# Kernel tuning notes

Hardware: AMD Instinct MI355X
Metric: run time of the kernel (lower is better)

## Reference

```python
import jax, jax.numpy as jnp
import numpy as np

N = 64000            # total nodes (64 graphs x 1000 nodes)
E = 1048576          # edges (~16 avg degree)
NB_NODES = 1000
NUM_GRAPHS = 64
F_IN, H1, H2, H3, OUT = 128, 256, 256, 128, 64


def setup_inputs() -> dict:
    key = jax.random.key(0)
    ks = jax.random.split(key, 12)
    x = jax.random.normal(ks[0], (N, F_IN), dtype=jnp.float32)
    # random edges within each graph: pick graph per edge, then local src/dst
    g = jax.random.randint(ks[1], (E,), 0, NUM_GRAPHS)
    src = g * NB_NODES + jax.random.randint(ks[2], (E,), 0, NB_NODES)
    dst = g * NB_NODES + jax.random.randint(ks[3], (E,), 0, NB_NODES)
    edge_index = jnp.stack([src, dst]).astype(jnp.int64)
    batch = (jnp.arange(N) // NB_NODES).astype(jnp.int64)  # sorted graph ids
    def glorot(k, fan_in, fan_out):
        s = jnp.sqrt(6.0 / (fan_in + fan_out))
        return jax.random.uniform(k, (fan_in, fan_out), jnp.float32, -s, s)
    return {
        "x": x, "edge_index": edge_index, "batch": batch,
        "W1": glorot(ks[4], F_IN, H1), "b1": jnp.zeros((H1,), jnp.float32),
        "W2": glorot(ks[5], H1, H2),   "b2": jnp.zeros((H2,), jnp.float32),
        "W3": glorot(ks[6], H2, H3),   "b3": jnp.zeros((H3,), jnp.float32),
        "Wfc": glorot(ks[7], H3 * NB_NODES, OUT),
        "bfc": jnp.zeros((OUT,), jnp.float32),
    }


def _gcn_norm(edge_index, n):
    # add self-loops, symmetric normalization D^-1/2 (A+I) D^-1/2
    loop = jnp.arange(n, dtype=edge_index.dtype)
    src = jnp.concatenate([edge_index[0], loop])
    dst = jnp.concatenate([edge_index[1], loop])
    deg = jax.ops.segment_sum(jnp.ones_like(src, jnp.float32), dst, num_segments=n)
    dinv = 1.0 / jnp.sqrt(deg)  # deg >= 1 thanks to self-loops
    norm = dinv[src] * dinv[dst]
    return src, dst, norm


def _gcn_layer(h, W, b, src, dst, norm, n):
    hl = h @ W                                   # [N, H]
    msg = hl[src] * norm[:, None]                # gather + scale
    agg = jax.ops.segment_sum(msg, dst, num_segments=n)  # scatter-add
    return agg + b


def reference(x, edge_index, batch, W1, b1, W2, b2, W3, b3, Wfc, bfc):
    n = x.shape[0]
    src, dst, norm = _gcn_norm(edge_index, n)
    h = jnp.tanh(_gcn_layer(x, W1, b1, src, dst, norm, n))
    h = jnp.tanh(_gcn_layer(h, W2, b2, src, dst, norm, n))
    h = jnp.tanh(_gcn_layer(h, W3, b3, src, dst, norm, n))
    # batch is sorted with equal graph sizes -> the per-graph loop/concat
    # in the original is exactly a reshape to [num_graphs, nodes*H3]
    h_concat = h.reshape(NUM_GRAPHS, NB_NODES * H3)
    return h_concat @ Wfc + bfc
```

## Files before the change

kernel.cpp:

```cpp
#include <hip/hip_runtime.h>
#include <math.h>

#define N_NODES 64000
#define N_EDGES 1048576
#define NB 1000
#define NG 64
#define NOUT 64
#define FC_SPLIT 500
#define BK_CAP 18000

typedef __attribute__((ext_vector_type(8))) short bfrag;
typedef __attribute__((ext_vector_type(4))) float f32x4;
typedef __attribute__((ext_vector_type(2))) float f32x2;

__device__ inline float bflo(unsigned int u) {
    union { unsigned int i; float f; } x; x.i = u << 16; return x.f;
}
__device__ inline float bfhi(unsigned int u) {
    union { unsigned int i; float f; } x; x.i = u & 0xffff0000u; return x.f;
}
__device__ inline f32x2 upk(unsigned int u) {
    f32x2 r; r.x = bflo(u); r.y = bfhi(u); return r;
}
__device__ inline unsigned short f2bf(float f) {
    union { float f; unsigned int i; } x; x.f = f;
    return (unsigned short)((x.i + 0x7FFFu + ((x.i >> 16) & 1u)) >> 16);
}
__device__ inline float tanh_fast(float x) {
    float e = __expf(2.0f * x);
    return fmaf(-2.0f, __builtin_amdgcn_rcpf(e + 1.0f), 1.0f);
}
__device__ inline int swz32(int row, int g) { return g ^ (row & 7) ^ (g >> 3); }
__device__ inline int swz16(int row, int g) { return g ^ (row & 7) ^ (g >> 3); }


__global__ __launch_bounds__(256) void k_bucket(const int* __restrict__ src,
                                                const int* __restrict__ dst,
                                                int* __restrict__ gcnt,
                                                unsigned int* __restrict__ bucket) {
    __shared__ int lcnt[64];
    __shared__ int lbase[64];
    __shared__ int lcur[64];
    int t = threadIdx.x;
    int e0 = blockIdx.x * 4096;
    if (t < 64) { lcnt[t] = 0; lcur[t] = 0; }
    __syncthreads();
    for (int i = t; i < 4096; i += 256) {
        int d = dst[e0 + i];
        int g = d / NB;
        atomicAdd(&lcnt[g], 1);
    }
    __syncthreads();
    if (t < 64) lbase[t] = atomicAdd(&gcnt[t], lcnt[t]);
    __syncthreads();
    for (int i = t; i < 4096; i += 256) {
        int d = dst[e0 + i];
        int s = src[e0 + i];
        int g = d / NB;
        int pos = atomicAdd(&lcur[g], 1);
        unsigned int packed = ((unsigned int)(d - g * NB) << 10) | (unsigned int)(s - g * NB);
        bucket[(size_t)g * BK_CAP + lbase[g] + pos] = packed;
    }
}

__global__ __launch_bounds__(1024) void k_build(const int* __restrict__ gcnt,
                                                const unsigned int* __restrict__ bucket,
                                                int* __restrict__ rowptr,
                                                int* __restrict__ rowend,
                                                float* __restrict__ dinv,
                                                unsigned short* __restrict__ colp) {
    __shared__ int ind[1024];
    __shared__ int tmp[1024];
    int t = threadIdx.x;
    int g = blockIdx.x;
    int cnt = gcnt[g];
    size_t base = (size_t)g * BK_CAP;
    ind[t] = 0;
    __syncthreads();
    for (int i = t; i < cnt; i += 1024) {
        unsigned int p = bucket[base + i];
        atomicAdd(&ind[p >> 10], 1);
    }
    __syncthreads();
    int deg = ind[t];
    if (t < NB) dinv[g * NB + t] = rsqrtf((float)(deg + 1));
    tmp[t] = deg;
    __syncthreads();
    for (int off = 1; off < 1024; off <<= 1) {
        int o = (t >= off) ? tmp[t - off] : 0;
        __syncthreads();
        tmp[t] += o;
        __syncthreads();
    }
    int excl = tmp[t] - deg;
    if (t < NB) {
        rowptr[g * NB + t] = (int)base + excl;
        rowend[g * NB + t] = (int)base + excl + deg;
    }
    ind[t] = excl;
    __syncthreads();
    for (int i = t; i < cnt; i += 1024) {
        unsigned int p = bucket[base + i];
        int dl = p >> 10;
        int pos = atomicAdd(&ind[dl], 1);
        colp[base + pos] = (unsigned short)(p & 1023u);
    }
}


__global__ void k_cast_scale(const float* __restrict__ in, const float* __restrict__ dinv,
                             unsigned short* __restrict__ out) {
    int i = (blockIdx.x * blockDim.x + threadIdx.x) * 4;
    float d = dinv[i >> 7];
    float4 v = *(const float4*)(in + i);
    union { unsigned short s[4]; uint2 u; } o;
    o.s[0] = f2bf(v.x * d); o.s[1] = f2bf(v.y * d);
    o.s[2] = f2bf(v.z * d); o.s[3] = f2bf(v.w * d);
    *(uint2*)(out + i) = o.u;
}

__global__ void k_wt_all(const float* __restrict__ W1, const float* __restrict__ W2,
                         const float* __restrict__ W3, unsigned short* __restrict__ W1t,
                         unsigned short* __restrict__ W2t, unsigned short* __restrict__ W3t) {
    int i = blockIdx.x * 256 + threadIdx.x;
    if (i < 32768) {
        int n = i / 128, k = i % 128;
        W1t[i] = f2bf(W1[k * 256 + n]);
    } else if (i < 98304) {
        int j = i - 32768;
        int n = j / 256, k = j % 256;
        W2t[j] = f2bf(W2[k * 256 + n]);
    } else {
        int j = i - 98304;
        int n = j / 256, k = j % 256;
        W3t[j] = f2bf(W3[k * 128 + n]);
    }
}


template <int H, bool TANH>
__global__ __launch_bounds__(256) void k_agg(const unsigned short* __restrict__ hs,
                                             unsigned short* __restrict__ op,
                                             const int* __restrict__ rowptr,
                                             const int* __restrict__ rowend,
                                             const unsigned short* __restrict__ col,
                                             const float* __restrict__ dinv,
                                             const float* __restrict__ bias) {
    constexpr int VEC = H / 64;
    int lane = threadIdx.x & 63;
    int b = blockIdx.x;
    int c = b & 7;
    int j = b >> 3;
    int g = c + 8 * (j / 250);
    int chunk = j % 250;
    int v = g * NB + chunk * 4 + (threadIdx.x >> 6);
    const unsigned short* gb = hs + (size_t)g * NB * H;
    f32x2 a0, a1;
    a0 = f32x2{0.f, 0.f}; a1 = f32x2{0.f, 0.f};
    {
        const unsigned short* r = hs + (size_t)v * H + lane * VEC;
        if (VEC == 2) {
            a0 = upk(*(const unsigned int*)r);
        } else {
            uint2 u = *(const uint2*)r;
            a0 = upk(u.x); a1 = upk(u.y);
        }
    }
    int beg = rowptr[v], end = rowend[v];
    for (int e0 = beg; e0 < end; e0 += 64) {
        int me = e0 + lane;
        int s = (me < end) ? (int)col[me] : 0;
        int cnt = min(64, end - e0);
        int i = 0;
        for (; i + 8 <= cnt; i += 8) {
            int sx[8];
#pragma unroll
            for (int q = 0; q < 8; ++q) sx[q] = __builtin_amdgcn_readlane(s, i + q);
            if (VEC == 2) {
                unsigned int u[8];
#pragma unroll
                for (int q = 0; q < 8; ++q)
                    u[q] = *(const unsigned int*)(gb + (size_t)sx[q] * H + lane * 2);
#pragma unroll
                for (int q = 0; q < 8; ++q) a0 += upk(u[q]);
            } else {
                uint2 u[8];
#pragma unroll
                for (int q = 0; q < 8; ++q)
                    u[q] = *(const uint2*)(gb + (size_t)sx[q] * H + lane * 4);
#pragma unroll
                for (int q = 0; q < 8; ++q) { a0 += upk(u[q].x); a1 += upk(u[q].y); }
            }
        }
        for (; i + 4 <= cnt; i += 4) {
            int sx[4];
#pragma unroll
            for (int q = 0; q < 4; ++q) sx[q] = __builtin_amdgcn_readlane(s, i + q);
            if (VEC == 2) {
                unsigned int u[4];
#pragma unroll
                for (int q = 0; q < 4; ++q)
                    u[q] = *(const unsigned int*)(gb + (size_t)sx[q] * H + lane * 2);
#pragma unroll
                for (int q = 0; q < 4; ++q) a0 += upk(u[q]);
            } else {
                uint2 u[4];
#pragma unroll
                for (int q = 0; q < 4; ++q)
                    u[q] = *(const uint2*)(gb + (size_t)sx[q] * H + lane * 4);
#pragma unroll
                for (int q = 0; q < 4; ++q) { a0 += upk(u[q].x); a1 += upk(u[q].y); }
            }
        }
        for (; i < cnt; ++i) {
            int ss = __builtin_amdgcn_readlane(s, i);
            if (VEC == 2) {
                a0 += upk(*(const unsigned int*)(gb + (size_t)ss * H + lane * 2));
            } else {
                uint2 u = *(const uint2*)(gb + (size_t)ss * H + lane * 4);
                a0 += upk(u.x); a1 += upk(u.y);
            }
        }
    }
    float dv = dinv[v];
    float acc[4];
    acc[0] = a0.x; acc[1] = a0.y;
    if (VEC == 4) { acc[2] = a1.x; acc[3] = a1.y; }
    if (TANH) {
#pragma unroll
        for (int q = 0; q < VEC; ++q) acc[q] = tanh_fast(acc[q] * dv + bias[lane * VEC + q]);
    } else {
#pragma unroll
        for (int q = 0; q < VEC; ++q) acc[q] *= dv;
    }
    unsigned short* o = op + (size_t)v * H + lane * VEC;
    if (VEC == 2) {
        union { unsigned short s[2]; unsigned int u; } pk;
        pk.s[0] = f2bf(acc[0]); pk.s[1] = f2bf(acc[1]);
        *(unsigned int*)o = pk.u;
    } else {
        union { unsigned short s[4]; uint2 u; } pk;
        pk.s[0] = f2bf(acc[0]); pk.s[1] = f2bf(acc[1]);
        pk.s[2] = f2bf(acc[2]); pk.s[3] = f2bf(acc[3]);
        *(uint2*)o = pk.u;
    }
}


__global__ __launch_bounds__(256, 4) void k_aggemm1(const unsigned short* __restrict__ P0,
                                                    const int* __restrict__ rowptr,
                                                    const int* __restrict__ rowend,
                                                    const unsigned short* __restrict__ col,
                                                    const float* __restrict__ dinv,
                                                    const unsigned short* __restrict__ W1t,
                                                    const float* __restrict__ b1,
                                                    unsigned short* __restrict__ C) {
    constexpr int K = 128, N = 256;
    __shared__ unsigned short at[32 * 128];
    int t = threadIdx.x;
    int w = t >> 6, l = t & 63;
    int lm = l & 15, lq = l >> 4;
    int n0 = w * 64;
    int row0 = lq * 4;
    int m0 = blockIdx.x * 32;

    for (int r = 0; r < 8; ++r) {
        int row = w * 8 + r;
        int v = m0 + row;
        int gv = v / NB;
        const unsigned short* gb = P0 + (size_t)gv * NB * K;
        f32x2 a0 = upk(*(const unsigned int*)(P0 + (size_t)v * K + l * 2));
        int beg = rowptr[v], end = rowend[v];
        for (int e0 = beg; e0 < end; e0 += 64) {
            int me = e0 + l;
            int s = (me < end) ? (int)col[me] : 0;
            int cnt = min(64, end - e0);
            int i = 0;
            for (; i + 8 <= cnt; i += 8) {
                int sx[8];
#pragma unroll
                for (int q = 0; q < 8; ++q) sx[q] = __builtin_amdgcn_readlane(s, i + q);
                unsigned int u[8];
#pragma unroll
                for (int q = 0; q < 8; ++q)
                    u[q] = *(const unsigned int*)(gb + (size_t)sx[q] * K + l * 2);
#pragma unroll
                for (int q = 0; q < 8; ++q) a0 += upk(u[q]);
            }
            for (; i + 4 <= cnt; i += 4) {
                int sx[4];
#pragma unroll
                for (int q = 0; q < 4; ++q) sx[q] = __builtin_amdgcn_readlane(s, i + q);
                unsigned int u[4];
#pragma unroll
                for (int q = 0; q < 4; ++q)
                    u[q] = *(const unsigned int*)(gb + (size_t)sx[q] * K + l * 2);
#pragma unroll
                for (int q = 0; q < 4; ++q) a0 += upk(u[q]);
            }
            for (; i < cnt; ++i) {
                int ss = __builtin_amdgcn_readlane(s, i);
                a0 += upk(*(const unsigned int*)(gb + (size_t)ss * K + l * 2));
            }
        }
        float dv = dinv[v];
        union { unsigned short s2[2]; unsigned int u; } pk;
        pk.s2[0] = f2bf(a0.x * dv); pk.s2[1] = f2bf(a0.y * dv);
        *(unsigned int*)&at[row * 128 + swz16(row, l >> 2) * 8 + (l & 3) * 2] = pk.u;
    }
    __syncthreads();

    f32x4 acc[2][4] = {};
    const unsigned short* Bb = W1t + (size_t)(n0 + lm) * K + lq * 8;
    bfrag bfb[2][4];
#pragma unroll
    for (int j = 0; j < 4; ++j) bfb[0][j] = *(const bfrag*)(Bb + (size_t)j * 16 * K);
#pragma unroll
    for (int it = 0; it < K / 32; ++it) {
        int ks = it * 32, cur = it & 1;
        if (it + 1 < K / 32) {
#pragma unroll
            for (int j = 0; j < 4; ++j)
                bfb[cur ^ 1][j] = *(const bfrag*)(Bb + (size_t)j * 16 * K + ks + 32);
        }
        bfrag af[2];
        int gidx = it * 4 + lq;
#pragma unroll
        for (int i = 0; i < 2; ++i) {
            int row = i * 16 + lm;
            af[i] = *(const bfrag*)&at[row * 128 + swz16(row, gidx) * 8];
        }
#pragma unroll
        for (int i = 0; i < 2; ++i)
#pragma unroll
            for (int j = 0; j < 4; ++j)
                acc[i][j] = __builtin_amdgcn_mfma_f32_16x16x32_bf16(af[i], bfb[cur][j], acc[i][j], 0, 0, 0);
    }
    float bj[4];
#pragma unroll
    for (int j = 0; j < 4; ++j) bj[j] = b1[n0 + j * 16 + lm];
    float drow[2][4];
#pragma unroll
    for (int i = 0; i < 2; ++i)
#pragma unroll
        for (int r = 0; r < 4; ++r) drow[i][r] = dinv[m0 + i * 16 + row0 + r];
#pragma unroll
    for (int i = 0; i < 2; ++i)
#pragma unroll
        for (int j = 0; j < 4; ++j)
#pragma unroll
            for (int r = 0; r < 4; ++r) {
                float v = tanh_fast(acc[i][j][r] + bj[j]) * drow[i][r];
                C[(size_t)(m0 + i * 16 + row0 + r) * N + n0 + j * 16 + lm] = f2bf(v);
            }
}


__global__ __launch_bounds__(256, 4) void k_aggemm23(const unsigned short* __restrict__ P2,
                                                     const int* __restrict__ rowptr,
                                                     const int* __restrict__ rowend,
                                                     const unsigned short* __restrict__ col,
                                                     const float* __restrict__ dinv,
                                                     const unsigned short* __restrict__ W2t,
                                                     const float* __restrict__ b2,
                                                     const unsigned short* __restrict__ W3t,
                                                     unsigned short* __restrict__ C) {
    constexpr int K = 256, N3 = 128;
    __shared__ unsigned short at[32 * 256];
    int t = threadIdx.x;
    int w = t >> 6, l = t & 63;
    int lm = l & 15, lq = l >> 4;
    int n0 = w * 64;
    int row0 = lq * 4;
    int m0 = blockIdx.x * 32;

    for (int r = 0; r < 8; ++r) {
        int row = w * 8 + r;
        int v = m0 + row;
        int gv = v / NB;
        const unsigned short* gb = P2 + (size_t)gv * NB * K;
        f32x2 a0, a1;
        {
            uint2 u = *(const uint2*)(P2 + (size_t)v * K + l * 4);
            a0 = upk(u.x); a1 = upk(u.y);
        }
        int beg = rowptr[v], end = rowend[v];
        for (int e0 = beg; e0 < end; e0 += 64) {
            int me = e0 + l;
            int s = (me < end) ? (int)col[me] : 0;
            int cnt = min(64, end - e0);
            int i = 0;
            for (; i + 8 <= cnt; i += 8) {
                int sx[8];
#pragma unroll
                for (int q = 0; q < 8; ++q) sx[q] = __builtin_amdgcn_readlane(s, i + q);
                uint2 u[8];
#pragma unroll
                for (int q = 0; q < 8; ++q)
                    u[q] = *(const uint2*)(gb + (size_t)sx[q] * K + l * 4);
#pragma unroll
                for (int q = 0; q < 8; ++q) { a0 += upk(u[q].x); a1 += upk(u[q].y); }
            }
            for (; i + 4 <= cnt; i += 4) {
                int sx[4];
#pragma unroll
                for (int q = 0; q < 4; ++q) sx[q] = __builtin_amdgcn_readlane(s, i + q);
                uint2 u[4];
#pragma unroll
                for (int q = 0; q < 4; ++q)
                    u[q] = *(const uint2*)(gb + (size_t)sx[q] * K + l * 4);
#pragma unroll
                for (int q = 0; q < 4; ++q) { a0 += upk(u[q].x); a1 += upk(u[q].y); }
            }
            for (; i < cnt; ++i) {
                int ss = __builtin_amdgcn_readlane(s, i);
                uint2 u = *(const uint2*)(gb + (size_t)ss * K + l * 4);
                a0 += upk(u.x); a1 += upk(u.y);
            }
        }
        float dv = dinv[v];
        union { unsigned short s4[4]; uint2 u; } pk;
        pk.s4[0] = f2bf(a0.x * dv); pk.s4[1] = f2bf(a0.y * dv);
        pk.s4[2] = f2bf(a1.x * dv); pk.s4[3] = f2bf(a1.y * dv);
        *(uint2*)&at[row * 256 + swz32(row, l >> 1) * 8 + (l & 1) * 4] = pk.u;
    }
    __syncthreads();

    f32x4 acc[2][4] = {};
    {
        const unsigned short* Bb = W2t + (size_t)(n0 + lm) * K + lq * 8;
        bfrag bfb[2][4];
#pragma unroll
        for (int j = 0; j < 4; ++j) bfb[0][j] = *(const bfrag*)(Bb + (size_t)j * 16 * K);
#pragma unroll
        for (int it = 0; it < K / 32; ++it) {
            int ks = it * 32, cur = it & 1;
            if (it + 1 < K / 32) {
#pragma unroll
                for (int j = 0; j < 4; ++j)
                    bfb[cur ^ 1][j] = *(const bfrag*)(Bb + (size_t)j * 16 * K + ks + 32);
            }
            bfrag af[2];
            int gidx = it * 4 + lq;
#pragma unroll
            for (int i = 0; i < 2; ++i) {
                int row = i * 16 + lm;
                af[i] = *(const bfrag*)&at[row * 256 + swz32(row, gidx) * 8];
            }
#pragma unroll
            for (int i = 0; i < 2; ++i)
#pragma unroll
                for (int j = 0; j < 4; ++j)
                    acc[i][j] = __builtin_amdgcn_mfma_f32_16x16x32_bf16(af[i], bfb[cur][j], acc[i][j], 0, 0, 0);
        }
    }
    __syncthreads();
    {
        float bj[4];
#pragma unroll
        for (int j = 0; j < 4; ++j) bj[j] = b2[n0 + j * 16 + lm];
#pragma unroll
        for (int i = 0; i < 2; ++i)
#pragma unroll
            for (int j = 0; j < 4; ++j) {
                int colb = n0 + j * 16 + lm;
                int gidx = colb >> 3, off = colb & 7;
#pragma unroll
                for (int r = 0; r < 4; ++r) {
                    int row = i * 16 + row0 + r;
                    at[row * 256 + swz32(row, gidx) * 8 + off] =
                        f2bf(tanh_fast(acc[i][j][r] + bj[j]));
                }
            }
    }
    __syncthreads();
    {
        f32x4 acc2[2][2] = {};
        int n3 = w * 32;
        const unsigned short* Bb = W3t + (size_t)(n3 + lm) * K + lq * 8;
        bfrag bfb[2][2];
#pragma unroll
        for (int j = 0; j < 2; ++j) bfb[0][j] = *(const bfrag*)(Bb + (size_t)j * 16 * K);
#pragma unroll
        for (int it = 0; it < K / 32; ++it) {
            int ks = it * 32, cur = it & 1;
            if (it + 1 < K / 32) {
#pragma unroll
                for (int j = 0; j < 2; ++j)
                    bfb[cur ^ 1][j] = *(const bfrag*)(Bb + (size_t)j * 16 * K + ks + 32);
            }
            bfrag af[2];
            int gidx = it * 4 + lq;
#pragma unroll
            for (int i = 0; i < 2; ++i) {
                int row = i * 16 + lm;
                af[i] = *(const bfrag*)&at[row * 256 + swz32(row, gidx) * 8];
            }
#pragma unroll
            for (int i = 0; i < 2; ++i)
#pragma unroll
                for (int j = 0; j < 2; ++j)
                    acc2[i][j] = __builtin_amdgcn_mfma_f32_16x16x32_bf16(af[i], bfb[cur][j], acc2[i][j], 0, 0, 0);
        }
        float drow[2][4];
#pragma unroll
        for (int i = 0; i < 2; ++i)
#pragma unroll
            for (int r = 0; r < 4; ++r) drow[i][r] = dinv[m0 + i * 16 + row0 + r];
#pragma unroll
        for (int i = 0; i < 2; ++i)
#pragma unroll
            for (int j = 0; j < 2; ++j)
#pragma unroll
                for (int r = 0; r < 4; ++r)
                    C[(size_t)(m0 + i * 16 + row0 + r) * N3 + n3 + j * 16 + lm] =
                        f2bf(acc2[i][j][r] * drow[i][r]);
    }
}


__global__ void k_fc(const unsigned short* __restrict__ A, const float* __restrict__ B,
                     float* __restrict__ part) {
    __shared__ float As[16][68];
    __shared__ float Bs[16][68];
    const int KROW = NB * 128;
    int t = threadIdx.x;
    int tx = t & 15, ty = t >> 4;
    int k0b = blockIdx.x * 256;
    float acc[4][4] = {};
    for (int k0 = k0b; k0 < k0b + 256; k0 += 16) {
        int arow = t >> 2, ak = (t & 3) << 2;
        uint2 ua = *(const uint2*)(A + (size_t)arow * KROW + k0 + ak);
        As[ak + 0][arow] = bflo(ua.x);
        As[ak + 1][arow] = bfhi(ua.x);
        As[ak + 2][arow] = bflo(ua.y);
        As[ak + 3][arow] = bfhi(ua.y);
        int bk = t >> 4, bn4 = (t & 15) << 2;
        *(float4*)&Bs[bk][bn4] = *(const float4*)(B + (size_t)(k0 + bk) * NOUT + bn4);
        __syncthreads();
#pragma unroll
        for (int kk = 0; kk < 16; ++kk) {
            float4 a = *(const float4*)&As[kk][ty << 2];
            float4 b = *(const float4*)&Bs[kk][tx << 2];
            acc[0][0] += a.x * b.x; acc[0][1] += a.x * b.y; acc[0][2] += a.x * b.z; acc[0][3] += a.x * b.w;
            acc[1][0] += a.y * b.x; acc[1][1] += a.y * b.y; acc[1][2] += a.y * b.z; acc[1][3] += a.y * b.w;
            acc[2][0] += a.z * b.x; acc[2][1] += a.z * b.y; acc[2][2] += a.z * b.z; acc[2][3] += a.z * b.w;
            acc[3][0] += a.w * b.x; acc[3][1] += a.w * b.y; acc[3][2] += a.w * b.z; acc[3][3] += a.w * b.w;
        }
        __syncthreads();
    }
    float* po = part + (size_t)blockIdx.x * (NG * NOUT);
#pragma unroll
    for (int i = 0; i < 4; ++i) {
        float4 r;
        r.x = acc[i][0]; r.y = acc[i][1]; r.z = acc[i][2]; r.w = acc[i][3];
        *(float4*)&po[((ty << 2) + i) * NOUT + (tx << 2)] = r;
    }
}

__global__ void k_fc_reduce(const float* __restrict__ part, const float* __restrict__ bfc,
                            float* __restrict__ out) {
    int i = blockIdx.x * blockDim.x + threadIdx.x;
    float s = bfc[i & 63];
    for (int b = 0; b < FC_SPLIT; ++b) s += part[(size_t)b * (NG * NOUT) + i];
    out[i] = s;
}


static inline size_t align256(size_t x) { return (x + 255) & ~(size_t)255; }

extern "C" void kernel_launch(void* const* d_in, const int* in_sizes, int n_in,
                              void* d_out, int out_size, void* d_ws, size_t ws_size,
                              hipStream_t stream) {
    const float* x   = (const float*)d_in[0];
    const int*   ei  = (const int*)d_in[1];
    const int*   src = ei;
    const int*   dst = ei + N_EDGES;
    const float* W1  = (const float*)d_in[3];
    const float* b1  = (const float*)d_in[4];
    const float* W2  = (const float*)d_in[5];
    const float* b2  = (const float*)d_in[6];
    const float* W3  = (const float*)d_in[7];
    const float* b3  = (const float*)d_in[8];
    const float* Wfc = (const float*)d_in[9];
    const float* bfc = (const float*)d_in[10];
    float* out = (float*)d_out;

    char* w = (char*)d_ws;
    unsigned short* P0 = (unsigned short*)w; w += align256((size_t)N_NODES * 256 * 2);
    unsigned short* P1 = (unsigned short*)w; w += align256((size_t)N_NODES * 256 * 2);
    unsigned short* P2 = (unsigned short*)w; w += align256((size_t)N_NODES * 256 * 2);
    int* rowptr = (int*)w;      w += align256((size_t)N_NODES * 4);
    int* rowend = (int*)w;      w += align256((size_t)N_NODES * 4);
    float* dinv = (float*)w;    w += align256((size_t)N_NODES * 4);
    int* gcnt = (int*)w;        w += align256((size_t)NG * 4);
    unsigned int* bucket = (unsigned int*)w; w += align256((size_t)NG * BK_CAP * 4);
    unsigned short* colp = (unsigned short*)w; w += align256((size_t)NG * BK_CAP * 2);
    float* fcpart = (float*)w;  w += align256((size_t)FC_SPLIT * NG * NOUT * 4);
    unsigned short* W1t = (unsigned short*)w; w += align256((size_t)128 * 256 * 2);
    unsigned short* W2t = (unsigned short*)w; w += align256((size_t)256 * 256 * 2);
    unsigned short* W3t = (unsigned short*)w; w += align256((size_t)256 * 128 * 2);

    hipMemsetAsync(gcnt, 0, (size_t)NG * 4, stream);
    k_bucket<<<N_EDGES / 4096, 256, 0, stream>>>(src, dst, gcnt, bucket);
    k_build<<<NG, 1024, 0, stream>>>(gcnt, bucket, rowptr, rowend, dinv, colp);

    k_cast_scale<<<(N_NODES * 128 / 4) / 256, 256, 0, stream>>>(x, dinv, P0);
    k_wt_all<<<512, 256, 0, stream>>>(W1, W2, W3, W1t, W2t, W3t);

    k_aggemm1<<<N_NODES / 32, 256, 0, stream>>>(P0, rowptr, rowend, colp, dinv, W1t, b1, P2);

    k_aggemm23<<<N_NODES / 32, 256, 0, stream>>>(P2, rowptr, rowend, colp, dinv, W2t, b2, W3t, P1);

    k_agg<128, true><<<N_NODES / 4, 256, 0, stream>>>(P1, P0, rowptr, rowend, colp, dinv, b3);

    k_fc<<<FC_SPLIT, 256, 0, stream>>>(P0, Wfc, fcpart);
    k_fc_reduce<<<NG * NOUT / 256, 256, 0, stream>>>(fcpart, bfc, out);
}
```

Measured before the change: 388.9 us.

## Remap aggregation-GEMM blocks so each graph's tiles share one XCD's L2

Block indices in the fused aggregate+GEMM kernels are remapped so that all 32-row chunks of a graph land on the same XCD (block index mod 8), and tiles no longer straddle graph boundaries. The goal is to keep a graph's feature rows, which are gathered repeatedly by neighbours, resident in that XCD's private L2 instead of spreading them across all eight L2s. The cost is padding: each graph uses 32 chunks of 32 rows, so the last chunk holds only 8 valid rows. This adds about 2.4% more blocks with masked rows and extra branching. The per-row graph-base computation is also hoisted.

```diff
diff --git a/kernel.cpp b/kernel.cpp
--- a/kernel.cpp
+++ b/kernel.cpp
@@ -247,6 +247,7 @@
 }
 
 
+
 __global__ __launch_bounds__(256, 4) void k_aggemm1(const unsigned short* __restrict__ P0,
                                                     const int* __restrict__ rowptr,
                                                     const int* __restrict__ rowend,
@@ -262,51 +263,60 @@
     int lm = l & 15, lq = l >> 4;
     int n0 = w * 64;
     int row0 = lq * 4;
-    int m0 = blockIdx.x * 32;
+    int b = blockIdx.x;
+    int xcd = b & 7, jj = b >> 3;
+    int g = xcd + 8 * (jj >> 5);
+    int chunk = jj & 31;
+    int m0 = g * NB + chunk * 32;
+    int nvalid = min(32, NB - chunk * 32);
+    const unsigned short* gb = P0 + (size_t)g * NB * K;
 
     for (int r = 0; r < 8; ++r) {
         int row = w * 8 + r;
-        int v = m0 + row;
-        int gv = v / NB;
-        const unsigned short* gb = P0 + (size_t)gv * NB * K;
-        f32x2 a0 = upk(*(const unsigned int*)(P0 + (size_t)v * K + l * 2));
-        int beg = rowptr[v], end = rowend[v];
-        for (int e0 = beg; e0 < end; e0 += 64) {
-            int me = e0 + l;
-            int s = (me < end) ? (int)col[me] : 0;
-            int cnt = min(64, end - e0);
-            int i = 0;
-            for (; i + 8 <= cnt; i += 8) {
-                int sx[8];
-#pragma unroll
-                for (int q = 0; q < 8; ++q) sx[q] = __builtin_amdgcn_readlane(s, i + q);
-                unsigned int u[8];
-#pragma unroll
-                for (int q = 0; q < 8; ++q)
-                    u[q] = *(const unsigned int*)(gb + (size_t)sx[q] * K + l * 2);
-#pragma unroll
-                for (int q = 0; q < 8; ++q) a0 += upk(u[q]);
-            }
-            for (; i + 4 <= cnt; i += 4) {
-                int sx[4];
-#pragma unroll
-                for (int q = 0; q < 4; ++q) sx[q] = __builtin_amdgcn_readlane(s, i + q);
-                unsigned int u[4];
-#pragma unroll
-                for (int q = 0; q < 4; ++q)
-                    u[q] = *(const unsigned int*)(gb + (size_t)sx[q] * K + l * 2);
-#pragma unroll
-                for (int q = 0; q < 4; ++q) a0 += upk(u[q]);
-            }
-            for (; i < cnt; ++i) {
-                int ss = __builtin_amdgcn_readlane(s, i);
-                a0 += upk(*(const unsigned int*)(gb + (size_t)ss * K + l * 2));
-            }
-        }
-        float dv = dinv[v];
-        union { unsigned short s2[2]; unsigned int u; } pk;
-        pk.s2[0] = f2bf(a0.x * dv); pk.s2[1] = f2bf(a0.y * dv);
-        *(unsigned int*)&at[row * 128 + swz16(row, l >> 2) * 8 + (l & 3) * 2] = pk.u;
+        unsigned int* slot = (unsigned int*)&at[row * 128 + swz16(row, l >> 2) * 8 + (l & 3) * 2];
+        if (row < nvalid) {
+            int v = m0 + row;
+            f32x2 a0 = upk(*(const unsigned int*)(P0 + (size_t)v * K + l * 2));
+            int beg = rowptr[v], end = rowend[v];
+            for (int e0 = beg; e0 < end; e0 += 64) {
+                int me = e0 + l;
+                int s = (me < end) ? (int)col[me] : 0;
+                int cnt = min(64, end - e0);
+                int i = 0;
+                for (; i + 8 <= cnt; i += 8) {
+                    int sx[8];
+#pragma unroll
+                    for (int q = 0; q < 8; ++q) sx[q] = __builtin_amdgcn_readlane(s, i + q);
+                    unsigned int u[8];
+#pragma unroll
+                    for (int q = 0; q < 8; ++q)
+                        u[q] = *(const unsigned int*)(gb + (size_t)sx[q] * K + l * 2);
+#pragma unroll
+                    for (int q = 0; q < 8; ++q) a0 += upk(u[q]);
+                }
+                for (; i + 4 <= cnt; i += 4) {
+                    int sx[4];
+#pragma unroll
+                    for (int q = 0; q < 4; ++q) sx[q] = __builtin_amdgcn_readlane(s, i + q);
+                    unsigned int u[4];
+#pragma unroll
+                    for (int q = 0; q < 4; ++q)
+                        u[q] = *(const unsigned int*)(gb + (size_t)sx[q] * K + l * 2);
+#pragma unroll
+                    for (int q = 0; q < 4; ++q) a0 += upk(u[q]);
+                }
+                for (; i < cnt; ++i) {
+                    int ss = __builtin_amdgcn_readlane(s, i);
+                    a0 += upk(*(const unsigned int*)(gb + (size_t)ss * K + l * 2));
+                }
+            }
+            float dv = dinv[v];
+            union { unsigned short s2[2]; unsigned int u; } pk;
+            pk.s2[0] = f2bf(a0.x * dv); pk.s2[1] = f2bf(a0.y * dv);
+            *slot = pk.u;
+        } else {
+            *slot = 0u;
+        }
     }
     __syncthreads();
 
@@ -339,20 +349,20 @@
     float bj[4];
 #pragma unroll
     for (int j = 0; j < 4; ++j) bj[j] = b1[n0 + j * 16 + lm];
-    float drow[2][4];
 #pragma unroll
     for (int i = 0; i < 2; ++i)
 #pragma unroll
-        for (int r = 0; r < 4; ++r) drow[i][r] = dinv[m0 + i * 16 + row0 + r];
-#pragma unroll
-    for (int i = 0; i < 2; ++i)
-#pragma unroll
-        for (int j = 0; j < 4; ++j)
-#pragma unroll
-            for (int r = 0; r < 4; ++r) {
-                float v = tanh_fast(acc[i][j][r] + bj[j]) * drow[i][r];
-                C[(size_t)(m0 + i * 16 + row0 + r) * N + n0 + j * 16 + lm] = f2bf(v);
-            }
+        for (int r = 0; r < 4; ++r) {
+            int rr = i * 16 + row0 + r;
+            if (rr < nvalid) {
+                float dv = dinv[m0 + rr];
+#pragma unroll
+                for (int j = 0; j < 4; ++j) {
+                    float v = tanh_fast(acc[i][j][r] + bj[j]) * dv;
+                    C[(size_t)(m0 + rr) * N + n0 + j * 16 + lm] = f2bf(v);
+                }
+            }
+        }
 }
 
 
@@ -372,57 +382,67 @@
     int lm = l & 15, lq = l >> 4;
     int n0 = w * 64;
     int row0 = lq * 4;
-    int m0 = blockIdx.x * 32;
+    int b = blockIdx.x;
+    int xcd = b & 7, jj = b >> 3;
+    int g = xcd + 8 * (jj >> 5);
+    int chunk = jj & 31;
+    int m0 = g * NB + chunk * 32;
+    int nvalid = min(32, NB - chunk * 32);
+    const unsigned short* gb = P2 + (size_t)g * NB * K;
 
     for (int r = 0; r < 8; ++r) {
         int row = w * 8 + r;
-        int v = m0 + row;
-        int gv = v / NB;
-        const unsigned short* gb = P2 + (size_t)gv * NB * K;
-        f32x2 a0, a1;
-        {
-            uint2 u = *(const uint2*)(P2 + (size_t)v * K + l * 4);
-            a0 = upk(u.x); a1 = upk(u.y);
-        }
-        int beg = rowptr[v], end = rowend[v];
-        for (int e0 = beg; e0 < end; e0 += 64) {
-            int me = e0 + l;
-            int s = (me < end) ? (int)col[me] : 0;
-            int cnt = min(64, end - e0);
-            int i = 0;
-            for (; i + 8 <= cnt; i += 8) {
-                int sx[8];
-#pragma unroll
-                for (int q = 0; q < 8; ++q) sx[q] = __builtin_amdgcn_readlane(s, i + q);
-                uint2 u[8];
-#pragma unroll
-                for (int q = 0; q < 8; ++q)
-                    u[q] = *(const uint2*)(gb + (size_t)sx[q] * K + l * 4);
-#pragma unroll
-                for (int q = 0; q < 8; ++q) { a0 += upk(u[q].x); a1 += upk(u[q].y); }
-            }
-            for (; i + 4 <= cnt; i += 4) {
-                int sx[4];
-#pragma unroll
-                for (int q = 0; q < 4; ++q) sx[q] = __builtin_amdgcn_readlane(s, i + q);
-                uint2 u[4];
-#pragma unroll
-                for (int q = 0; q < 4; ++q)
-                    u[q] = *(const uint2*)(gb + (size_t)sx[q] * K + l * 4);
-#pragma unroll
-                for (int q = 0; q < 4; ++q) { a0 += upk(u[q].x); a1 += upk(u[q].y); }
-            }
-            for (; i < cnt; ++i) {
-                int ss = __builtin_amdgcn_readlane(s, i);
-                uint2 u = *(const uint2*)(gb + (size_t)ss * K + l * 4);
-                a0 += upk(u.x); a1 += upk(u.y);
-            }
-        }
-        float dv = dinv[v];
-        union { unsigned short s4[4]; uint2 u; } pk;
-        pk.s4[0] = f2bf(a0.x * dv); pk.s4[1] = f2bf(a0.y * dv);
-        pk.s4[2] = f2bf(a1.x * dv); pk.s4[3] = f2bf(a1.y * dv);
-        *(uint2*)&at[row * 256 + swz32(row, l >> 1) * 8 + (l & 1) * 4] = pk.u;
+        uint2* slot = (uint2*)&at[row * 256 + swz32(row, l >> 1) * 8 + (l & 1) * 4];
+        if (row < nvalid) {
+            int v = m0 + row;
+            f32x2 a0, a1;
+            {
+                uint2 u = *(const uint2*)(P2 + (size_t)v * K + l * 4);
+                a0 = upk(u.x); a1 = upk(u.y);
+            }
+            int beg = rowptr[v], end = rowend[v];
+            for (int e0 = beg; e0 < end; e0 += 64) {
+                int me = e0 + l;
+                int s = (me < end) ? (int)col[me] : 0;
+                int cnt = min(64, end - e0);
+                int i = 0;
+                for (; i + 8 <= cnt; i += 8) {
+                    int sx[8];
+#pragma unroll
+                    for (int q = 0; q < 8; ++q) sx[q] = __builtin_amdgcn_readlane(s, i + q);
+                    uint2 u[8];
+#pragma unroll
+                    for (int q = 0; q < 8; ++q)
+                        u[q] = *(const uint2*)(gb + (size_t)sx[q] * K + l * 4);
+#pragma unroll
+                    for (int q = 0; q < 8; ++q) { a0 += upk(u[q].x); a1 += upk(u[q].y); }
+                }
+                for (; i + 4 <= cnt; i += 4) {
+                    int sx[4];
+#pragma unroll
+                    for (int q = 0; q < 4; ++q) sx[q] = __builtin_amdgcn_readlane(s, i + q);
+                    uint2 u[4];
+#pragma unroll
+                    for (int q = 0; q < 4; ++q)
+                        u[q] = *(const uint2*)(gb + (size_t)sx[q] * K + l * 4);
+#pragma unroll
+                    for (int q = 0; q < 4; ++q) { a0 += upk(u[q].x); a1 += upk(u[q].y); }
+                }
+                for (; i < cnt; ++i) {
+                    int ss = __builtin_amdgcn_readlane(s, i);
+                    uint2 u = *(const uint2*)(gb + (size_t)ss * K + l * 4);
+                    a0 += upk(u.x); a1 += upk(u.y);
+                }
+            }
+            float dv = dinv[v];
+            union { unsigned short s4[4]; uint2 u; } pk;
+            pk.s4[0] = f2bf(a0.x * dv); pk.s4[1] = f2bf(a0.y * dv);
+            pk.s4[2] = f2bf(a1.x * dv); pk.s4[3] = f2bf(a1.y * dv);
+            *slot = pk.u;
+        } else {
+            uint2 z; z.x = 0u; z.y = 0u;
+            *slot = z;
+        }
     }
     __syncthreads();
 
@@ -502,19 +522,20 @@
                 for (int j = 0; j < 2; ++j)
                     acc2[i][j] = __builtin_amdgcn_mfma_f32_16x16x32_bf16(af[i], bfb[cur][j], acc2[i][j], 0, 0, 0);
         }
-        float drow[2][4];
+        int n3b = w * 32;
 #pragma unroll
         for (int i = 0; i < 2; ++i)
 #pragma unroll
-            for (int r = 0; r < 4; ++r) drow[i][r] = dinv[m0 + i * 16 + row0 + r];
-#pragma unroll
-        for (int i = 0; i < 2; ++i)
-#pragma unroll
-            for (int j = 0; j < 2; ++j)
-#pragma unroll
-                for (int r = 0; r < 4; ++r)
-                    C[(size_t)(m0 + i * 16 + row0 + r) * N3 + n3 + j * 16 + lm] =
-                        f2bf(acc2[i][j][r] * drow[i][r]);
+            for (int r = 0; r < 4; ++r) {
+                int rr = i * 16 + row0 + r;
+                if (rr < nvalid) {
+                    float dv = dinv[m0 + rr];
+#pragma unroll
+                    for (int j = 0; j < 2; ++j)
+                        C[(size_t)(m0 + rr) * N3 + n3b + j * 16 + lm] =
+                            f2bf(acc2[i][j][r] * dv);
+                }
+            }
     }
 }
 
@@ -608,9 +629,9 @@
     k_cast_scale<<<(N_NODES * 128 / 4) / 256, 256, 0, stream>>>(x, dinv, P0);
     k_wt_all<<<512, 256, 0, stream>>>(W1, W2, W3, W1t, W2t, W3t);
 
-    k_aggemm1<<<N_NODES / 32, 256, 0, stream>>>(P0, rowptr, rowend, colp, dinv, W1t, b1, P2);
-
-    k_aggemm23<<<N_NODES / 32, 256, 0, stream>>>(P2, rowptr, rowend, colp, dinv, W2t, b2, W3t, P1);
+    k_aggemm1<<<NG * 32, 256, 0, stream>>>(P0, rowptr, rowend, colp, dinv, W1t, b1, P2);
+
+    k_aggemm23<<<NG * 32, 256, 0, stream>>>(P2, rowptr, rowend, colp, dinv, W2t, b2, W3t, P1);
 
     k_agg<128, true><<<N_NODES / 4, 256, 0, stream>>>(P1, P0, rowptr, rowend, colp, dinv, b3);
 
```

Result: faster. 357.2 us (-8.2%).
